# Performance work log

Measured on AMD Instinct MI355X. Metric: run time of the kernel, lower is better.

## Reference

```python
import jax, jax.numpy as jnp
import numpy as np

D = 2048        # dim
H = 16          # n_heads
FFN = 4 * D     # ffn hidden
K = 8192        # working-memory slots
HID = 32        # halt-gate hidden
EPS = 1e-5      # LayerNorm eps


def setup_inputs() -> dict:
    key = jax.random.key(0)
    ks = jax.random.split(key, 16)
    s = 0.02  # weight init scale for numerical sanity
    def rn(k, shape, scale=s):
        return jax.random.normal(k, shape, dtype=jnp.float32) * scale
    return {
        "workspace": jax.random.normal(ks[0], (D,), dtype=jnp.float32),
        "wm_context": jax.random.normal(ks[1], (K, D), dtype=jnp.float32),
        "self_in_w": rn(ks[2], (3 * D, D)), "self_in_b": jnp.zeros((3 * D,), jnp.float32),
        "self_out_w": rn(ks[3], (D, D)), "self_out_b": jnp.zeros((D,), jnp.float32),
        "cross_in_w": rn(ks[4], (3 * D, D)), "cross_in_b": jnp.zeros((3 * D,), jnp.float32),
        "cross_out_w": rn(ks[5], (D, D)), "cross_out_b": jnp.zeros((D,), jnp.float32),
        "ffn_w1": rn(ks[6], (FFN, D)), "ffn_b1": jnp.zeros((FFN,), jnp.float32),
        "ffn_w2": rn(ks[7], (D, FFN)), "ffn_b2": jnp.zeros((D,), jnp.float32),
        "ln1_g": jnp.ones((D,), jnp.float32), "ln1_b": jnp.zeros((D,), jnp.float32),
        "ln2_g": jnp.ones((D,), jnp.float32), "ln2_b": jnp.zeros((D,), jnp.float32),
        "ln3_g": jnp.ones((D,), jnp.float32), "ln3_b": jnp.zeros((D,), jnp.float32),
        "halt_w1": rn(ks[8], (HID, D)), "halt_b1": jnp.zeros((HID,), jnp.float32),
        "halt_w2": rn(ks[9], (1, HID)), "halt_b2": jnp.zeros((1,), jnp.float32),
        "max_steps": 5,
    }


def _ln(x, g, b):
    m = x.mean()
    v = jnp.mean((x - m) ** 2)
    return (x - m) / jnp.sqrt(v + EPS) * g + b


def _mha(xq, xkv, in_w, in_b, out_w, out_b):
    # xq: (D,) single query token; xkv: (L, D) keys/values. Eval mode (no dropout).
    d = xq.shape[-1]
    hd = d // H
    wq, wk, wv = in_w[:d], in_w[d:2 * d], in_w[2 * d:]
    bq, bk, bv = in_b[:d], in_b[d:2 * d], in_b[2 * d:]
    q = (xq @ wq.T + bq).reshape(H, hd)            # (H, hd)
    k = (xkv @ wk.T + bk).reshape(-1, H, hd)       # (L, H, hd)
    v = (xkv @ wv.T + bv).reshape(-1, H, hd)       # (L, H, hd)
    scores = jnp.einsum("hd,khd->hk", q, k) * (hd ** -0.5)  # (H, L)
    attn = jax.nn.softmax(scores, axis=-1)
    o = jnp.einsum("hk,khd->hd", attn, v).reshape(d)
    return o @ out_w.T + out_b


def reference(workspace, wm_context,
              self_in_w, self_in_b, self_out_w, self_out_b,
              cross_in_w, cross_in_b, cross_out_w, cross_out_b,
              ffn_w1, ffn_b1, ffn_w2, ffn_b2,
              ln1_g, ln1_b, ln2_g, ln2_b, ln3_g, ln3_b,
              halt_w1, halt_b1, halt_w2, halt_b2, max_steps):
    state = workspace
    cum = jnp.float32(0.0)
    acc = jnp.zeros_like(state)
    active = jnp.bool_(True)
    for _ in range(max_steps):  # fixed small loop over ACT steps
        cross = _mha(state, wm_context, cross_in_w, cross_in_b, cross_out_w, cross_out_b)
        s1 = _ln(state + cross, ln1_g, ln1_b)
        sa = _mha(s1, s1[None, :], self_in_w, self_in_b, self_out_w, self_out_b)
        s2 = _ln(s1 + sa, ln2_g, ln2_b)
        h = jax.nn.gelu(s2 @ ffn_w1.T + ffn_b1, approximate=False)
        new_state = _ln(s2 + (h @ ffn_w2.T + ffn_b2), ln3_g, ln3_b)
        hh = jax.nn.gelu(new_state @ halt_w1.T + halt_b1, approximate=False)
        halt = jax.nn.sigmoid(hh @ halt_w2.T + halt_b2)[0]
        new_cum = cum + halt
        halts = new_cum >= 1.0 - 1e-6
        # remainder = 1 - cum_before if halting, else halt_prob
        w = jnp.where(halts, 1.0 - cum, halt)
        acc = acc + jnp.where(active, w, 0.0) * new_state
        state = jnp.where(active, new_state, state)
        cum = jnp.where(active, new_cum, cum)
        active = jnp.logical_and(active, jnp.logical_not(halts))
    # if loop exhausted without halting, add leftover mass on last state
    acc = acc + jnp.where(cum < 1.0 - 1e-6, 1.0 - cum, 0.0) * state
    return acc
```

## Files before the change

kernel.cpp:

```cpp
#include <hip/hip_runtime.h>
#include <math.h>

#define DD 2048
#define NH 16
#define HDIM 128
#define NK 8192
#define NFFN 8192
#define NHID 32
#define EPSV 1e-5f

typedef __attribute__((ext_vector_type(8))) short bf16x8;
typedef __attribute__((ext_vector_type(4))) float f32x4;

static const size_t W_ST  = 0;
static const size_t W_AC  = 2048;
static const size_t W_SC  = 4096;
static const size_t W_Q   = 4160;
static const size_t W_T   = 6208;
static const size_t W_TB  = 38976;
static const size_t W_PS  = 55360;
static const size_t W_P   = 1103936;
static const size_t W_PB  = 1235008;
static const size_t W_U   = 1300544;
static const size_t W_O   = 1333312;
static const size_t W_CR  = 1335360;
static const size_t W_S1  = 1337408;
static const size_t W_V   = 1339456;
static const size_t W_SA  = 1341504;
static const size_t W_S2  = 1343552;
static const size_t W_H1  = 1345600;
static const size_t W_F2  = 1353792;
static const size_t W_NS  = 1355840;
static const size_t W_PUA = 1357888;
static const size_t W_PUB = 1882176;
static const size_t W_WMB = 1882176;
static const size_t W_WMT = 10270784;
static const size_t W_ENDA  = 18659392;
static const size_t W_ENDB  = 6076480;
static const size_t W_ENDB2 = 2930752;

__device__ __forceinline__ float gelu_exact(float x) {
  return 0.5f * x * (1.0f + erff(x * 0.70710678118654752f));
}
__device__ __forceinline__ unsigned short f2bf(float x) {
  unsigned u = __float_as_uint(x);
  u += 0x7FFFu + ((u >> 16) & 1u);
  return (unsigned short)(u >> 16);
}

__global__ void init_kernel(const float* __restrict__ w0, float* __restrict__ state,
                            float* __restrict__ acc, float* __restrict__ scal) {
  int i = blockIdx.x * 256 + threadIdx.x;
  if (i < DD) { state[i] = w0[i]; acc[i] = 0.f; }
  if (i == 0) { scal[0] = 0.f; scal[1] = 1.f; }
}

__global__ void prep_wm(const float* __restrict__ wm, unsigned short* __restrict__ wmb,
                        unsigned short* __restrict__ wmbT) {
  __shared__ unsigned short tile[64][72];
  int bk = blockIdx.x & 127, bc = blockIdx.x >> 7;
  int k0 = bk * 64, c0 = bc * 64;
  int tx = threadIdx.x & 15, ty = threadIdx.x >> 4;
#pragma unroll
  for (int rr = 0; rr < 4; ++rr) {
    int r = ty + rr * 16;
    float4 v = *reinterpret_cast<const float4*>(wm + (size_t)(k0 + r) * DD + c0 + tx * 4);
    ushort4 u4;
    u4.x = f2bf(v.x); u4.y = f2bf(v.y); u4.z = f2bf(v.z); u4.w = f2bf(v.w);
    *reinterpret_cast<ushort4*>(wmb + (size_t)(k0 + r) * DD + c0 + tx * 4) = u4;
    tile[tx * 4 + 0][r] = u4.x; tile[tx * 4 + 1][r] = u4.y;
    tile[tx * 4 + 2][r] = u4.z; tile[tx * 4 + 3][r] = u4.w;
  }
  __syncthreads();
#pragma unroll
  for (int rr = 0; rr < 4; ++rr) {
    int c = ty + rr * 16;
    ushort4 o;
    o.x = tile[c][tx * 4]; o.y = tile[c][tx * 4 + 1];
    o.z = tile[c][tx * 4 + 2]; o.w = tile[c][tx * 4 + 3];
    *reinterpret_cast<ushort4*>(wmbT + (size_t)(c0 + c) * NK + k0 + tx * 4) = o;
  }
}

__global__ void matvec_kernel(const float* __restrict__ W, const float* __restrict__ bias,
                              const float* __restrict__ x, float* __restrict__ y,
                              int R, int C, int act, int perhead,
                              const float* __restrict__ scal, int gated) {
  if (gated && scal[1] == 0.f) return;
  int wid = threadIdx.x >> 6, lane = threadIdx.x & 63;
  int row = blockIdx.x * 4 + wid;
  if (row >= R) return;
  const float* w = W + (size_t)row * C;
  const float* xv = perhead ? (x + (size_t)(row >> 7) * C) : x;
  float acc = 0.f;
  for (int c = lane * 4; c < C; c += 64 * 4) {
    float4 wv = *reinterpret_cast<const float4*>(w + c);
    float4 xx = *reinterpret_cast<const float4*>(xv + c);
    acc += wv.x * xx.x + wv.y * xx.y + wv.z * xx.z + wv.w * xx.w;
  }
  for (int off = 32; off > 0; off >>= 1) acc += __shfl_xor(acc, off, 64);
  if (lane == 0) {
    float r = acc + bias[row];
    if (act == 1) r = gelu_exact(r);
    y[row] = r;
  }
}

__global__ void tproj_kernel(const float* __restrict__ Wk, const float* __restrict__ q,
                             float* __restrict__ t, unsigned short* __restrict__ tb,
                             int obf, const float* __restrict__ scal) {
  if (scal[1] == 0.f) return;
  int h = blockIdx.x >> 4;
  int ct = blockIdx.x & 15;
  int c = ct * 128 + threadIdx.x;
  const float* wb = Wk + (size_t)(h * HDIM) * DD + c;
  const float* qh = q + h * HDIM;
  float acc = 0.f;
  for (int d = 0; d < HDIM; ++d) acc += qh[d] * wb[(size_t)d * DD];
  if (obf) tb[h * DD + c] = f2bf(acc);
  else     t[h * DD + c] = acc;
}

__global__ __launch_bounds__(256, 4) void scores_mfma(const unsigned short* __restrict__ wmb,
                                                      const unsigned short* __restrict__ tb,
                                                      float* __restrict__ part_s,
                                                      const float* __restrict__ scal) {
  if (scal[1] == 0.f) return;
  int w = threadIdx.x >> 6, lane = threadIdx.x & 63;
  int task = blockIdx.x * 4 + w;
  int cc = task & 7, rg = task >> 3;
  int r0 = rg * 16, c0 = cc * 256;
  int l15 = lane & 15, kg = lane >> 4;
  const unsigned short* ap = wmb + (size_t)(r0 + l15) * DD + c0 + kg * 8;
  const unsigned short* bp = tb + (size_t)l15 * DD + c0 + kg * 8;
  bf16x8 a[8], b[8];
#pragma unroll
  for (int i = 0; i < 8; ++i) {
    a[i] = *reinterpret_cast<const bf16x8*>(ap + i * 32);
    b[i] = *reinterpret_cast<const bf16x8*>(bp + i * 32);
  }
  f32x4 acc = {0.f, 0.f, 0.f, 0.f};
#pragma unroll
  for (int i = 0; i < 8; ++i)
    acc = __builtin_amdgcn_mfma_f32_16x16x32_bf16(a[i], b[i], acc, 0, 0, 0);
  float* op = part_s + ((size_t)cc * NH + l15) * NK + r0 + kg * 4;
#pragma unroll
  for (int r = 0; r < 4; ++r) op[r] = acc[r];
}

__global__ __launch_bounds__(256, 4) void u_mfma(const unsigned short* __restrict__ wmbT,
                                                 const unsigned short* __restrict__ pb,
                                                 float* __restrict__ part_u,
                                                 const float* __restrict__ scal) {
  if (scal[1] == 0.f) return;
  int w = threadIdx.x >> 6, lane = threadIdx.x & 63;
  int task = blockIdx.x * 4 + w;
  int ct = task & 127, kc = task >> 7;
  int c0 = ct * 16, k0 = kc * 512;
  int l15 = lane & 15, kg = lane >> 4;
  const unsigned short* ap = pb + (size_t)l15 * NK + k0 + kg * 8;
  const unsigned short* bp = wmbT + (size_t)(c0 + l15) * NK + k0 + kg * 8;
  f32x4 acc = {0.f, 0.f, 0.f, 0.f};
#pragma unroll
  for (int half = 0; half < 2; ++half) {
    bf16x8 a[8], b[8];
#pragma unroll
    for (int i = 0; i < 8; ++i) {
      a[i] = *reinterpret_cast<const bf16x8*>(ap + half * 256 + i * 32);
      b[i] = *reinterpret_cast<const bf16x8*>(bp + half * 256 + i * 32);
    }
#pragma unroll
    for (int i = 0; i < 8; ++i)
      acc = __builtin_amdgcn_mfma_f32_16x16x32_bf16(a[i], b[i], acc, 0, 0, 0);
  }
  float* op = part_u + ((size_t)kc * NH + kg * 4) * DD + c0 + l15;
#pragma unroll
  for (int r = 0; r < 4; ++r) op[(size_t)r * DD] = acc[r];
}

#define FMA16(wvv, tp)                                                       \
  {                                                                          \
    float4 t0 = tp[0], t1 = tp[1], t2 = tp[2], t3 = tp[3];                   \
    acc[0] += wvv * t0.x; acc[1] += wvv * t0.y;                              \
    acc[2] += wvv * t0.z; acc[3] += wvv * t0.w;                              \
    acc[4] += wvv * t1.x; acc[5] += wvv * t1.y;                              \
    acc[6] += wvv * t1.z; acc[7] += wvv * t1.w;                              \
    acc[8] += wvv * t2.x; acc[9] += wvv * t2.y;                              \
    acc[10] += wvv * t2.z; acc[11] += wvv * t2.w;                            \
    acc[12] += wvv * t3.x; acc[13] += wvv * t3.y;                            \
    acc[14] += wvv * t3.z; acc[15] += wvv * t3.w;                            \
  }

__global__ void scores_kernel(const float* __restrict__ wm, const float* __restrict__ t,
                              float* __restrict__ part_s, const float* __restrict__ scal) {
  if (scal[1] == 0.f) return;
  int kt = blockIdx.x >> 3;
  int cc = blockIdx.x & 7;
  int tid = threadIdx.x;
  int k0 = kt * 128, c0 = cc * 256;
  __shared__ float wlds[128 * 33];
  __shared__ float tlds[256 * 20];
  for (int j = 0; j < 32; ++j) {
    int idx = j * 128 + tid;
    int h = idx >> 8, c = idx & 255;
    tlds[c * 20 + h] = t[(size_t)h * DD + c0 + c];
  }
  float acc[NH];
#pragma unroll
  for (int h = 0; h < NH; ++h) acc[h] = 0.f;
  for (int s = 0; s < 8; ++s) {
    int cbase = c0 + s * 32;
    __syncthreads();
    for (int p = 0; p < 8; ++p) {
      int f = p * 128 + tid;
      int r = f >> 3, fc = f & 7;
      float4 v = *reinterpret_cast<const float4*>(wm + (size_t)(k0 + r) * DD + cbase + fc * 4);
      float* d = wlds + r * 33 + fc * 4;
      d[0] = v.x; d[1] = v.y; d[2] = v.z; d[3] = v.w;
    }
    __syncthreads();
    const float* myrow = wlds + tid * 33;
#pragma unroll 4
    for (int cb = 0; cb < 32; ++cb) {
      float wvv = myrow[cb];
      const float4* tp = reinterpret_cast<const float4*>(tlds + (size_t)(s * 32 + cb) * 20);
      FMA16(wvv, tp);
    }
  }
#pragma unroll
  for (int h = 0; h < NH; ++h)
    part_s[((size_t)cc * NH + h) * NK + k0 + tid] = acc[h];
}

__global__ void softmax_kernel(const float* __restrict__ part_s, float* __restrict__ p,
                               unsigned short* __restrict__ pb, int obf,
                               const float* __restrict__ scal) {
  if (scal[1] == 0.f) return;
  int h = blockIdx.x;
  int tid = threadIdx.x;
  __shared__ float red[256];
  float v[32];
  float mx = -1e30f;
  for (int j = 0; j < 32; ++j) {
    int k = tid + j * 256;
    float s = 0.f;
    for (int cc = 0; cc < 8; ++cc) s += part_s[((size_t)cc * NH + h) * NK + k];
    s *= 0.08838834764831845f;
    v[j] = s;
    mx = fmaxf(mx, s);
  }
  red[tid] = mx; __syncthreads();
  for (int off = 128; off > 0; off >>= 1) { if (tid < off) red[tid] = fmaxf(red[tid], red[tid + off]); __syncthreads(); }
  mx = red[0]; __syncthreads();
  float sum = 0.f;
  for (int j = 0; j < 32; ++j) { v[j] = expf(v[j] - mx); sum += v[j]; }
  red[tid] = sum; __syncthreads();
  for (int off = 128; off > 0; off >>= 1) { if (tid < off) red[tid] += red[tid + off]; __syncthreads(); }
  float inv = 1.f / red[0];
  for (int j = 0; j < 32; ++j) {
    float val = v[j] * inv;
    size_t idx = (size_t)h * NK + tid + j * 256;
    if (obf) pb[idx] = f2bf(val);
    else     p[idx] = val;
  }
}

#define U1FMA(i, ph) \
  acc[i].x += w4.x * (ph); acc[i].y += w4.y * (ph); \
  acc[i].z += w4.z * (ph); acc[i].w += w4.w * (ph);

template <int KCH>
__global__ void u1_kernel(const float* __restrict__ wm, const float* __restrict__ p,
                          float* __restrict__ part_u, const float* __restrict__ scal) {
  if (scal[1] == 0.f) return;
  int kc = blockIdx.x >> 2;
  int ct = blockIdx.x & 3;
  int tid = threadIdx.x;
  int k0 = kc * KCH;
  int c = ct * 512 + tid * 4;
  __shared__ float plds[KCH * 16];
  for (int j = 0; j < KCH * 16 / 128; ++j) {
    int idx = j * 128 + tid;
    int h = idx / KCH, k = idx % KCH;
    plds[k * 16 + h] = p[(size_t)h * NK + k0 + k];
  }
  __syncthreads();
  float4 acc[NH];
#pragma unroll
  for (int h = 0; h < NH; ++h) acc[h] = make_float4(0.f, 0.f, 0.f, 0.f);
#pragma unroll 2
  for (int k = 0; k < KCH; ++k) {
    float4 w4 = *reinterpret_cast<const float4*>(wm + (size_t)(k0 + k) * DD + c);
    const float4* pp = reinterpret_cast<const float4*>(plds + k * 16);
    float4 p0 = pp[0], p1 = pp[1], p2 = pp[2], p3 = pp[3];
    U1FMA(0, p0.x)  U1FMA(1, p0.y)  U1FMA(2, p0.z)  U1FMA(3, p0.w)
    U1FMA(4, p1.x)  U1FMA(5, p1.y)  U1FMA(6, p1.z)  U1FMA(7, p1.w)
    U1FMA(8, p2.x)  U1FMA(9, p2.y)  U1FMA(10, p2.z) U1FMA(11, p2.w)
    U1FMA(12, p3.x) U1FMA(13, p3.y) U1FMA(14, p3.z) U1FMA(15, p3.w)
  }
#pragma unroll
  for (int h = 0; h < NH; ++h)
    *reinterpret_cast<float4*>(part_u + ((size_t)kc * NH + h) * DD + c) = acc[h];
}

__global__ void u2_kernel(const float* __restrict__ part_u, float* __restrict__ u,
                          const float* __restrict__ scal, int nkc) {
  if (scal[1] == 0.f) return;
  int i = blockIdx.x * 256 + threadIdx.x;
  float s = 0.f;
  for (int kc = 0; kc < nkc; ++kc) s += part_u[(size_t)kc * NH * DD + i];
  u[i] = s;
}

__global__ void ln_kernel(const float* __restrict__ a, const float* __restrict__ r,
                          const float* __restrict__ g, const float* __restrict__ beta,
                          float* __restrict__ out, const float* __restrict__ scal) {
  if (scal[1] == 0.f) return;
  __shared__ float red[256];
  __shared__ float mv[2];
  int tid = threadIdx.x;
  float x[8];
  float s = 0.f;
  for (int j = 0; j < 8; ++j) { int i = tid * 8 + j; x[j] = a[i] + r[i]; s += x[j]; }
  red[tid] = s; __syncthreads();
  for (int off = 128; off > 0; off >>= 1) { if (tid < off) red[tid] += red[tid + off]; __syncthreads(); }
  if (tid == 0) mv[0] = red[0] * (1.f / DD);
  __syncthreads();
  float m = mv[0];
  s = 0.f;
  for (int j = 0; j < 8; ++j) { float d = x[j] - m; s += d * d; }
  red[tid] = s; __syncthreads();
  for (int off = 128; off > 0; off >>= 1) { if (tid < off) red[tid] += red[tid + off]; __syncthreads(); }
  if (tid == 0) mv[1] = 1.f / sqrtf(red[0] * (1.f / DD) + EPSV);
  __syncthreads();
  float inv = mv[1];
  for (int j = 0; j < 8; ++j) { int i = tid * 8 + j; out[i] = (x[j] - m) * inv * g[i] + beta[i]; }
}

__global__ void act_kernel(const float* __restrict__ hw1, const float* __restrict__ hb1,
                           const float* __restrict__ hw2, const float* __restrict__ hb2,
                           const float* __restrict__ ns, float* __restrict__ state,
                           float* __restrict__ acc, float* __restrict__ scal,
                           const int* __restrict__ max_steps, int step) {
  if (step >= max_steps[0]) return;
  if (scal[1] == 0.f) return;
  __shared__ float red[NHID][9];
  __shared__ float hh[NHID];
  __shared__ float wbc;
  int tid = threadIdx.x;
  int row = tid >> 3, seg = tid & 7;
  const float* wr = hw1 + (size_t)row * DD + seg * 256;
  const float* nsp = ns + seg * 256;
  float s = 0.f;
  for (int i = 0; i < 256; ++i) s += wr[i] * nsp[i];
  red[row][seg] = s; __syncthreads();
  if (tid < NHID) {
    float t = hb1[tid];
    for (int j = 0; j < 8; ++j) t += red[tid][j];
    hh[tid] = gelu_exact(t);
  }
  __syncthreads();
  if (tid == 0) {
    float hs = hb2[0];
    for (int j = 0; j < NHID; ++j) hs += hh[j] * hw2[j];
    float halt = 1.f / (1.f + expf(-hs));
    float cum = scal[0];
    float ncum = cum + halt;
    int halts = (ncum >= 1.f - 1e-6f);
    wbc = halts ? (1.f - cum) : halt;
    scal[0] = ncum;
    scal[1] = halts ? 0.f : 1.f;
  }
  __syncthreads();
  float w = wbc;
  for (int i = tid; i < DD; i += 256) {
    acc[i] += w * ns[i];
    state[i] = ns[i];
  }
}

__global__ void final_kernel(const float* __restrict__ state, const float* __restrict__ acc,
                             const float* __restrict__ scal, float* __restrict__ out) {
  float cum = scal[0];
  float w = (cum < 1.f - 1e-6f) ? (1.f - cum) : 0.f;
  int i = blockIdx.x * 256 + threadIdx.x;
  if (i < DD) out[i] = acc[i] + w * state[i];
}

extern "C" void kernel_launch(void* const* d_in, const int* in_sizes, int n_in,
                              void* d_out, int out_size, void* d_ws, size_t ws_size,
                              hipStream_t stream) {
  const float* workspace   = (const float*)d_in[0];
  const float* wm          = (const float*)d_in[1];
  const float* self_in_w   = (const float*)d_in[2];
  const float* self_in_b   = (const float*)d_in[3];
  const float* self_out_w  = (const float*)d_in[4];
  const float* self_out_b  = (const float*)d_in[5];
  const float* cross_in_w  = (const float*)d_in[6];
  const float* cross_in_b  = (const float*)d_in[7];
  const float* cross_out_w = (const float*)d_in[8];
  const float* cross_out_b = (const float*)d_in[9];
  const float* ffn_w1      = (const float*)d_in[10];
  const float* ffn_b1      = (const float*)d_in[11];
  const float* ffn_w2      = (const float*)d_in[12];
  const float* ffn_b2      = (const float*)d_in[13];
  const float* ln1_g = (const float*)d_in[14];
  const float* ln1_b = (const float*)d_in[15];
  const float* ln2_g = (const float*)d_in[16];
  const float* ln2_b = (const float*)d_in[17];
  const float* ln3_g = (const float*)d_in[18];
  const float* ln3_b = (const float*)d_in[19];
  const float* halt_w1 = (const float*)d_in[20];
  const float* halt_b1 = (const float*)d_in[21];
  const float* halt_w2 = (const float*)d_in[22];
  const float* halt_b2 = (const float*)d_in[23];
  const int*   max_steps = (const int*)d_in[24];

  float* ws = (float*)d_ws;
  float* out = (float*)d_out;

  float* ST = ws + W_ST;  float* AC = ws + W_AC;  float* SC = ws + W_SC;
  float* Q_ = ws + W_Q;   float* T_ = ws + W_T;   float* PS = ws + W_PS;
  float* P_ = ws + W_P;   float* U_ = ws + W_U;   float* O_ = ws + W_O;
  float* CR = ws + W_CR;  float* S1 = ws + W_S1;  float* V_ = ws + W_V;
  float* SA = ws + W_SA;  float* S2 = ws + W_S2;  float* H1 = ws + W_H1;
  float* F2 = ws + W_F2;  float* NS = ws + W_NS;
  float* PUA = ws + W_PUA;
  float* PUB = ws + W_PUB;
  unsigned short* TB  = (unsigned short*)(ws + W_TB);
  unsigned short* PB  = (unsigned short*)(ws + W_PB);
  unsigned short* WMB = (unsigned short*)(ws + W_WMB);
  unsigned short* WMT = (unsigned short*)(ws + W_WMT);

  const bool tierA = W_ENDA * sizeof(float) <= ws_size;
  const bool bigB  = W_ENDB * sizeof(float) <= ws_size;

  init_kernel<<<8, 256, 0, stream>>>(workspace, ST, AC, SC);
  if (tierA) prep_wm<<<4096, 256, 0, stream>>>(wm, WMB, WMT);

  for (int s = 0; s < 5; ++s) {
    matvec_kernel<<<512, 256, 0, stream>>>(cross_in_w, cross_in_b, ST, Q_, DD, DD, 0, 0, SC, 1);
    tproj_kernel<<<256, 128, 0, stream>>>(cross_in_w + (size_t)DD * DD, Q_, T_, TB,
                                          tierA ? 1 : 0, SC);
    if (tierA) {
      scores_mfma<<<1024, 256, 0, stream>>>(WMB, TB, PS, SC);
      softmax_kernel<<<16, 256, 0, stream>>>(PS, P_, PB, 1, SC);
      u_mfma<<<512, 256, 0, stream>>>(WMT, PB, PUA, SC);
      u2_kernel<<<128, 256, 0, stream>>>(PUA, U_, SC, 16);
    } else {
      scores_kernel<<<512, 128, 0, stream>>>(wm, T_, PS, SC);
      softmax_kernel<<<16, 256, 0, stream>>>(PS, P_, PB, 0, SC);
      if (bigB) u1_kernel<64><<<512, 128, 0, stream>>>(wm, P_, PUB, SC);
      else      u1_kernel<256><<<128, 128, 0, stream>>>(wm, P_, PUB, SC);
      u2_kernel<<<128, 256, 0, stream>>>(PUB, U_, SC, bigB ? 128 : 32);
    }
    matvec_kernel<<<512, 256, 0, stream>>>(cross_in_w + (size_t)2 * DD * DD, cross_in_b + 2 * DD,
                                           U_, O_, DD, DD, 0, 1, SC, 1);
    matvec_kernel<<<512, 256, 0, stream>>>(cross_out_w, cross_out_b, O_, CR, DD, DD, 0, 0, SC, 1);
    ln_kernel<<<1, 256, 0, stream>>>(ST, CR, ln1_g, ln1_b, S1, SC);
    matvec_kernel<<<512, 256, 0, stream>>>(self_in_w + (size_t)2 * DD * DD, self_in_b + 2 * DD,
                                           S1, V_, DD, DD, 0, 0, SC, 1);
    matvec_kernel<<<512, 256, 0, stream>>>(self_out_w, self_out_b, V_, SA, DD, DD, 0, 0, SC, 1);
    ln_kernel<<<1, 256, 0, stream>>>(S1, SA, ln2_g, ln2_b, S2, SC);
    matvec_kernel<<<2048, 256, 0, stream>>>(ffn_w1, ffn_b1, S2, H1, NFFN, DD, 1, 0, SC, 1);
    matvec_kernel<<<512, 256, 0, stream>>>(ffn_w2, ffn_b2, H1, F2, DD, NFFN, 0, 0, SC, 1);
    ln_kernel<<<1, 256, 0, stream>>>(S2, F2, ln3_g, ln3_b, NS, SC);
    act_kernel<<<1, 256, 0, stream>>>(halt_w1, halt_b1, halt_w2, halt_b2, NS, ST, AC, SC,
                                      max_steps, s);
  }
  final_kernel<<<8, 256, 0, stream>>>(ST, AC, SC, out);
}
```

Baseline: 413.7 us.

## Fuse LayerNorms and partial-sum reductions into neighbouring matvec kernels

```diff
diff --git a/kernel.cpp b/kernel.cpp
--- a/kernel.cpp
+++ b/kernel.cpp
@@ -37,7 +37,6 @@
 static const size_t W_WMT = 10270784;
 static const size_t W_ENDA  = 18659392;
 static const size_t W_ENDB  = 6076480;
-static const size_t W_ENDB2 = 2930752;
 
 __device__ __forceinline__ float gelu_exact(float x) {
   return 0.5f * x * (1.0f + erff(x * 0.70710678118654752f));
@@ -46,6 +45,46 @@
   unsigned u = __float_as_uint(x);
   u += 0x7FFFu + ((u >> 16) & 1u);
   return (unsigned short)(u >> 16);
+}
+
+__device__ __forceinline__ float wave_dot(const float* __restrict__ w, const float* x, int C) {
+  int lane = threadIdx.x & 63;
+  float acc = 0.f;
+  for (int c = lane * 4; c < C; c += 256) {
+    float4 wv = *reinterpret_cast<const float4*>(w + c);
+    float4 xx = *reinterpret_cast<const float4*>(x + c);
+    acc += wv.x * xx.x + wv.y * xx.y + wv.z * xx.z + wv.w * xx.w;
+  }
+#pragma unroll
+  for (int off = 32; off; off >>= 1) acc += __shfl_xor(acc, off, 64);
+  return acc;
+}
+
+__device__ void block_ln(const float* x1, const float* x2,
+                         const float* __restrict__ g, const float* __restrict__ be,
+                         float* o, float* red) {
+  int tid = threadIdx.x;
+  float loc[8]; float s = 0.f;
+#pragma unroll
+  for (int j = 0; j < 8; ++j) { int i = tid * 8 + j; float v = x1[i] + x2[i]; loc[j] = v; s += v; }
+#pragma unroll
+  for (int off = 32; off; off >>= 1) s += __shfl_xor(s, off, 64);
+  __syncthreads();
+  if ((tid & 63) == 0) red[tid >> 6] = s;
+  __syncthreads();
+  float m = (red[0] + red[1] + red[2] + red[3]) * (1.f / 2048.f);
+  s = 0.f;
+#pragma unroll
+  for (int j = 0; j < 8; ++j) { float d = loc[j] - m; s += d * d; }
+#pragma unroll
+  for (int off = 32; off; off >>= 1) s += __shfl_xor(s, off, 64);
+  __syncthreads();
+  if ((tid & 63) == 0) red[tid >> 6] = s;
+  __syncthreads();
+  float inv = 1.f / sqrtf((red[0] + red[1] + red[2] + red[3]) * (1.f / 2048.f) + EPSV);
+#pragma unroll
+  for (int j = 0; j < 8; ++j) { int i = tid * 8 + j; o[i] = (loc[j] - m) * inv * g[i] + be[i]; }
+  __syncthreads();
 }
 
 __global__ void init_kernel(const float* __restrict__ w0, float* __restrict__ state,
@@ -93,7 +132,7 @@
   const float* w = W + (size_t)row * C;
   const float* xv = perhead ? (x + (size_t)(row >> 7) * C) : x;
   float acc = 0.f;
-  for (int c = lane * 4; c < C; c += 64 * 4) {
+  for (int c = lane * 4; c < C; c += 256) {
     float4 wv = *reinterpret_cast<const float4*>(w + c);
     float4 xx = *reinterpret_cast<const float4*>(xv + c);
     acc += wv.x * xx.x + wv.y * xx.y + wv.z * xx.z + wv.w * xx.w;
@@ -110,8 +149,7 @@
                              float* __restrict__ t, unsigned short* __restrict__ tb,
                              int obf, const float* __restrict__ scal) {
   if (scal[1] == 0.f) return;
-  int h = blockIdx.x >> 4;
-  int ct = blockIdx.x & 15;
+  int h = blockIdx.x >> 4, ct = blockIdx.x & 15;
   int c = ct * 128 + threadIdx.x;
   const float* wb = Wk + (size_t)(h * HDIM) * DD + c;
   const float* qh = q + h * HDIM;
@@ -177,6 +215,161 @@
 #pragma unroll
   for (int r = 0; r < 4; ++r) op[(size_t)r * DD] = acc[r];
 }
+
+__global__ void softmax_kernel(const float* __restrict__ part_s, float* __restrict__ p,
+                               unsigned short* __restrict__ pb, int obf,
+                               const float* __restrict__ scal) {
+  if (scal[1] == 0.f) return;
+  int h = blockIdx.x, tid = threadIdx.x;
+  __shared__ float red[256];
+  float v[32]; float mx = -1e30f;
+  for (int j = 0; j < 32; ++j) {
+    int k = tid + j * 256; float s = 0.f;
+    for (int cc = 0; cc < 8; ++cc) s += part_s[((size_t)cc * NH + h) * NK + k];
+    s *= 0.08838834764831845f;
+    v[j] = s; mx = fmaxf(mx, s);
+  }
+  red[tid] = mx; __syncthreads();
+  for (int off = 128; off > 0; off >>= 1) { if (tid < off) red[tid] = fmaxf(red[tid], red[tid + off]); __syncthreads(); }
+  mx = red[0]; __syncthreads();
+  float sum = 0.f;
+  for (int j = 0; j < 32; ++j) { v[j] = expf(v[j] - mx); sum += v[j]; }
+  red[tid] = sum; __syncthreads();
+  for (int off = 128; off > 0; off >>= 1) { if (tid < off) red[tid] += red[tid + off]; __syncthreads(); }
+  float inv = 1.f / red[0];
+  for (int j = 0; j < 32; ++j) {
+    float val = v[j] * inv;
+    size_t idx = (size_t)h * NK + tid + j * 256;
+    if (obf) pb[idx] = f2bf(val);
+    else     p[idx] = val;
+  }
+}
+
+__global__ __launch_bounds__(256) void o_fused_kernel(const float* __restrict__ part_u,
+                                                      const float* __restrict__ Wv,
+                                                      const float* __restrict__ bv,
+                                                      float* __restrict__ O,
+                                                      const float* __restrict__ scal) {
+  if (scal[1] == 0.f) return;
+  __shared__ float uh[2048];
+  int tid = threadIdx.x, wid = tid >> 6, lane = tid & 63;
+  int h = blockIdx.x >> 5;
+#pragma unroll
+  for (int j = 0; j < 8; ++j) {
+    int c = tid + j * 256;
+    float ss = 0.f;
+#pragma unroll
+    for (int kc = 0; kc < 16; ++kc) ss += part_u[((size_t)kc * NH + h) * DD + c];
+    uh[c] = ss;
+  }
+  __syncthreads();
+  int row = h * HDIM + (blockIdx.x & 31) * 4 + wid;
+  float a = wave_dot(Wv + (size_t)row * DD, uh, DD);
+  if (lane == 0) O[row] = a + bv[row];
+}
+
+__global__ __launch_bounds__(256) void v_ln1_kernel(const float* __restrict__ ST,
+                                                    const float* __restrict__ CR,
+                                                    const float* __restrict__ g1,
+                                                    const float* __restrict__ b1,
+                                                    const float* __restrict__ W,
+                                                    const float* __restrict__ bias,
+                                                    float* __restrict__ V,
+                                                    const float* __restrict__ scal) {
+  if (scal[1] == 0.f) return;
+  __shared__ float s1[2048];
+  __shared__ float red[8];
+  block_ln(ST, CR, g1, b1, s1, red);
+  int wid = threadIdx.x >> 6, lane = threadIdx.x & 63;
+  int row = blockIdx.x * 4 + wid;
+  float a = wave_dot(W + (size_t)row * DD, s1, DD);
+  if (lane == 0) V[row] = a + bias[row];
+}
+
+__global__ __launch_bounds__(256) void ffn1_kernel(const float* __restrict__ ST,
+                                                   const float* __restrict__ CR,
+                                                   const float* __restrict__ SA,
+                                                   const float* __restrict__ g1,
+                                                   const float* __restrict__ b1,
+                                                   const float* __restrict__ g2,
+                                                   const float* __restrict__ b2,
+                                                   const float* __restrict__ W,
+                                                   const float* __restrict__ bias,
+                                                   float* __restrict__ H1,
+                                                   const float* __restrict__ scal) {
+  if (scal[1] == 0.f) return;
+  __shared__ float s1[2048];
+  __shared__ float s2[2048];
+  __shared__ float red[8];
+  block_ln(ST, CR, g1, b1, s1, red);
+  block_ln(s1, SA, g2, b2, s2, red);
+  int wid = threadIdx.x >> 6, lane = threadIdx.x & 63;
+  int gw = blockIdx.x * 4 + wid;
+  for (int r = gw; r < NFFN; r += 2048) {
+    float a = wave_dot(W + (size_t)r * DD, s2, DD);
+    if (lane == 0) H1[r] = gelu_exact(a + bias[r]);
+  }
+}
+
+__global__ void act_ln3_kernel(const float* __restrict__ ST, const float* __restrict__ CR,
+                               const float* __restrict__ SA, const float* __restrict__ F2,
+                               const float* __restrict__ g1, const float* __restrict__ b1,
+                               const float* __restrict__ g2, const float* __restrict__ b2,
+                               const float* __restrict__ g3, const float* __restrict__ b3,
+                               const float* __restrict__ hw1, const float* __restrict__ hb1,
+                               const float* __restrict__ hw2, const float* __restrict__ hb2,
+                               float* __restrict__ state, float* __restrict__ acc,
+                               float* __restrict__ scal, const int* __restrict__ max_steps,
+                               int step) {
+  if (step >= max_steps[0]) return;
+  if (scal[1] == 0.f) return;
+  __shared__ float sA[2048];
+  __shared__ float sB[2048];
+  __shared__ float red[8];
+  __shared__ float hh[NHID];
+  __shared__ float wbc;
+  int tid = threadIdx.x;
+  block_ln(ST, CR, g1, b1, sA, red);
+  block_ln(sA, SA, g2, b2, sB, red);
+  block_ln(sB, F2, g3, b3, sA, red);
+  int row = tid >> 3, seg = tid & 7;
+  const float* wr = hw1 + (size_t)row * DD + seg * 256;
+  const float* np = sA + seg * 256;
+  float s = 0.f;
+  for (int i = 0; i < 256; ++i) s += wr[i] * np[i];
+  sB[row * 8 + seg] = s;
+  __syncthreads();
+  if (tid < NHID) {
+    float t2 = hb1[tid];
+#pragma unroll
+    for (int j = 0; j < 8; ++j) t2 += sB[tid * 8 + j];
+    hh[tid] = gelu_exact(t2);
+  }
+  __syncthreads();
+  if (tid == 0) {
+    float hs = hb2[0];
+    for (int j = 0; j < NHID; ++j) hs += hh[j] * hw2[j];
+    float halt = 1.f / (1.f + expf(-hs));
+    float cum = scal[0];
+    float ncum = cum + halt;
+    int halts = (ncum >= 1.f - 1e-6f);
+    wbc = halts ? (1.f - cum) : halt;
+    scal[0] = ncum;
+    scal[1] = halts ? 0.f : 1.f;
+  }
+  __syncthreads();
+  float w = wbc;
+  for (int i = tid; i < DD; i += 256) { acc[i] += w * sA[i]; state[i] = sA[i]; }
+}
+
+__global__ void final_kernel(const float* __restrict__ state, const float* __restrict__ acc,
+                             const float* __restrict__ scal, float* __restrict__ out) {
+  float cum = scal[0];
+  float w = (cum < 1.f - 1e-6f) ? (1.f - cum) : 0.f;
+  int i = blockIdx.x * 256 + threadIdx.x;
+  if (i < DD) out[i] = acc[i] + w * state[i];
+}
+
 
 #define FMA16(wvv, tp)                                                       \
   {                                                                          \
@@ -194,8 +387,7 @@
 __global__ void scores_kernel(const float* __restrict__ wm, const float* __restrict__ t,
                               float* __restrict__ part_s, const float* __restrict__ scal) {
   if (scal[1] == 0.f) return;
-  int kt = blockIdx.x >> 3;
-  int cc = blockIdx.x & 7;
+  int kt = blockIdx.x >> 3, cc = blockIdx.x & 7;
   int tid = threadIdx.x;
   int k0 = kt * 128, c0 = cc * 256;
   __shared__ float wlds[128 * 33];
@@ -208,8 +400,8 @@
   float acc[NH];
 #pragma unroll
   for (int h = 0; h < NH; ++h) acc[h] = 0.f;
-  for (int s = 0; s < 8; ++s) {
-    int cbase = c0 + s * 32;
+  for (int sl = 0; sl < 8; ++sl) {
+    int cbase = c0 + sl * 32;
     __syncthreads();
     for (int p = 0; p < 8; ++p) {
       int f = p * 128 + tid;
@@ -223,46 +415,13 @@
 #pragma unroll 4
     for (int cb = 0; cb < 32; ++cb) {
       float wvv = myrow[cb];
-      const float4* tp = reinterpret_cast<const float4*>(tlds + (size_t)(s * 32 + cb) * 20);
+      const float4* tp = reinterpret_cast<const float4*>(tlds + (size_t)(sl * 32 + cb) * 20);
       FMA16(wvv, tp);
     }
   }
 #pragma unroll
   for (int h = 0; h < NH; ++h)
     part_s[((size_t)cc * NH + h) * NK + k0 + tid] = acc[h];
-}
-
-__global__ void softmax_kernel(const float* __restrict__ part_s, float* __restrict__ p,
-                               unsigned short* __restrict__ pb, int obf,
-                               const float* __restrict__ scal) {
-  if (scal[1] == 0.f) return;
-  int h = blockIdx.x;
-  int tid = threadIdx.x;
-  __shared__ float red[256];
-  float v[32];
-  float mx = -1e30f;
-  for (int j = 0; j < 32; ++j) {
-    int k = tid + j * 256;
-    float s = 0.f;
-    for (int cc = 0; cc < 8; ++cc) s += part_s[((size_t)cc * NH + h) * NK + k];
-    s *= 0.08838834764831845f;
-    v[j] = s;
-    mx = fmaxf(mx, s);
-  }
-  red[tid] = mx; __syncthreads();
-  for (int off = 128; off > 0; off >>= 1) { if (tid < off) red[tid] = fmaxf(red[tid], red[tid + off]); __syncthreads(); }
-  mx = red[0]; __syncthreads();
-  float sum = 0.f;
-  for (int j = 0; j < 32; ++j) { v[j] = expf(v[j] - mx); sum += v[j]; }
-  red[tid] = sum; __syncthreads();
-  for (int off = 128; off > 0; off >>= 1) { if (tid < off) red[tid] += red[tid + off]; __syncthreads(); }
-  float inv = 1.f / red[0];
-  for (int j = 0; j < 32; ++j) {
-    float val = v[j] * inv;
-    size_t idx = (size_t)h * NK + tid + j * 256;
-    if (obf) pb[idx] = f2bf(val);
-    else     p[idx] = val;
-  }
 }
 
 #define U1FMA(i, ph) \
@@ -273,8 +432,7 @@
 __global__ void u1_kernel(const float* __restrict__ wm, const float* __restrict__ p,
                           float* __restrict__ part_u, const float* __restrict__ scal) {
   if (scal[1] == 0.f) return;
-  int kc = blockIdx.x >> 2;
-  int ct = blockIdx.x & 3;
+  int kc = blockIdx.x >> 2, ct = blockIdx.x & 3;
   int tid = threadIdx.x;
   int k0 = kc * KCH;
   int c = ct * 512 + tid * 4;
@@ -319,15 +477,13 @@
   __shared__ float red[256];
   __shared__ float mv[2];
   int tid = threadIdx.x;
-  float x[8];
-  float s = 0.f;
+  float x[8]; float s = 0.f;
   for (int j = 0; j < 8; ++j) { int i = tid * 8 + j; x[j] = a[i] + r[i]; s += x[j]; }
   red[tid] = s; __syncthreads();
   for (int off = 128; off > 0; off >>= 1) { if (tid < off) red[tid] += red[tid + off]; __syncthreads(); }
   if (tid == 0) mv[0] = red[0] * (1.f / DD);
   __syncthreads();
-  float m = mv[0];
-  s = 0.f;
+  float m = mv[0]; s = 0.f;
   for (int j = 0; j < 8; ++j) { float d = x[j] - m; s += d * d; }
   red[tid] = s; __syncthreads();
   for (int off = 128; off > 0; off >>= 1) { if (tid < off) red[tid] += red[tid + off]; __syncthreads(); }
@@ -373,18 +529,7 @@
   }
   __syncthreads();
   float w = wbc;
-  for (int i = tid; i < DD; i += 256) {
-    acc[i] += w * ns[i];
-    state[i] = ns[i];
-  }
-}
-
-__global__ void final_kernel(const float* __restrict__ state, const float* __restrict__ acc,
-                             const float* __restrict__ scal, float* __restrict__ out) {
-  float cum = scal[0];
-  float w = (cum < 1.f - 1e-6f) ? (1.f - cum) : 0.f;
-  int i = blockIdx.x * 256 + threadIdx.x;
-  if (i < DD) out[i] = acc[i] + w * state[i];
+  for (int i = tid; i < DD; i += 256) { acc[i] += w * ns[i]; state[i] = ns[i]; }
 }
 
 extern "C" void kernel_launch(void* const* d_in, const int* in_sizes, int n_in,
@@ -420,53 +565,67 @@
   float* out = (float*)d_out;
 
   float* ST = ws + W_ST;  float* AC = ws + W_AC;  float* SC = ws + W_SC;
-  float* Q_ = ws + W_Q;   float* T_ = ws + W_T;   float* PS = ws + W_PS;
-  float* P_ = ws + W_P;   float* U_ = ws + W_U;   float* O_ = ws + W_O;
-  float* CR = ws + W_CR;  float* S1 = ws + W_S1;  float* V_ = ws + W_V;
-  float* SA = ws + W_SA;  float* S2 = ws + W_S2;  float* H1 = ws + W_H1;
-  float* F2 = ws + W_F2;  float* NS = ws + W_NS;
-  float* PUA = ws + W_PUA;
-  float* PUB = ws + W_PUB;
+  float* Q_ = ws + W_Q;   float* PS = ws + W_PS;  float* O_ = ws + W_O;
+  float* CR = ws + W_CR;  float* V_ = ws + W_V;   float* SA = ws + W_SA;
+  float* H1 = ws + W_H1;  float* F2 = ws + W_F2;  float* PU = ws + W_PUA;
   unsigned short* TB  = (unsigned short*)(ws + W_TB);
   unsigned short* PB  = (unsigned short*)(ws + W_PB);
   unsigned short* WMB = (unsigned short*)(ws + W_WMB);
   unsigned short* WMT = (unsigned short*)(ws + W_WMT);
 
   const bool tierA = W_ENDA * sizeof(float) <= ws_size;
-  const bool bigB  = W_ENDB * sizeof(float) <= ws_size;
 
   init_kernel<<<8, 256, 0, stream>>>(workspace, ST, AC, SC);
-  if (tierA) prep_wm<<<4096, 256, 0, stream>>>(wm, WMB, WMT);
-
-  for (int s = 0; s < 5; ++s) {
-    matvec_kernel<<<512, 256, 0, stream>>>(cross_in_w, cross_in_b, ST, Q_, DD, DD, 0, 0, SC, 1);
-    tproj_kernel<<<256, 128, 0, stream>>>(cross_in_w + (size_t)DD * DD, Q_, T_, TB,
-                                          tierA ? 1 : 0, SC);
-    if (tierA) {
+
+  if (tierA) {
+    prep_wm<<<4096, 256, 0, stream>>>(wm, WMB, WMT);
+    for (int s = 0; s < 5; ++s) {
+      matvec_kernel<<<512, 256, 0, stream>>>(cross_in_w, cross_in_b, ST, Q_, DD, DD, 0, 0, SC, 1);
+      tproj_kernel<<<256, 128, 0, stream>>>(cross_in_w + (size_t)DD * DD, Q_, nullptr, TB, 1, SC);
       scores_mfma<<<1024, 256, 0, stream>>>(WMB, TB, PS, SC);
-      softmax_kernel<<<16, 256, 0, stream>>>(PS, P_, PB, 1, SC);
-      u_mfma<<<512, 256, 0, stream>>>(WMT, PB, PUA, SC);
-      u2_kernel<<<128, 256, 0, stream>>>(PUA, U_, SC, 16);
-    } else {
+      softmax_kernel<<<16, 256, 0, stream>>>(PS, nullptr, PB, 1, SC);
+      u_mfma<<<512, 256, 0, stream>>>(WMT, PB, PU, SC);
+      o_fused_kernel<<<512, 256, 0, stream>>>(PU, cross_in_w + (size_t)2 * DD * DD,
+                                              cross_in_b + 2 * DD, O_, SC);
+      matvec_kernel<<<512, 256, 0, stream>>>(cross_out_w, cross_out_b, O_, CR, DD, DD, 0, 0, SC, 1);
+      v_ln1_kernel<<<512, 256, 0, stream>>>(ST, CR, ln1_g, ln1_b,
+                                            self_in_w + (size_t)2 * DD * DD,
+                                            self_in_b + 2 * DD, V_, SC);
+      matvec_kernel<<<512, 256, 0, stream>>>(self_out_w, self_out_b, V_, SA, DD, DD, 0, 0, SC, 1);
+      ffn1_kernel<<<512, 256, 0, stream>>>(ST, CR, SA, ln1_g, ln1_b, ln2_g, ln2_b,
+                                           ffn_w1, ffn_b1, H1, SC);
+      matvec_kernel<<<512, 256, 0, stream>>>(ffn_w2, ffn_b2, H1, F2, DD, NFFN, 0, 0, SC, 1);
+      act_ln3_kernel<<<1, 256, 0, stream>>>(ST, CR, SA, F2, ln1_g, ln1_b, ln2_g, ln2_b,
+                                            ln3_g, ln3_b, halt_w1, halt_b1, halt_w2, halt_b2,
+                                            ST, AC, SC, max_steps, s);
+    }
+  } else {
+    float* T_ = ws + W_T;   float* P_ = ws + W_P;   float* U_ = ws + W_U;
+    float* S1 = ws + W_S1;  float* S2 = ws + W_S2;  float* NS = ws + W_NS;
+    float* PUB = ws + W_PUB;
+    const bool bigB = W_ENDB * sizeof(float) <= ws_size;
+    for (int s = 0; s < 5; ++s) {
+      matvec_kernel<<<512, 256, 0, stream>>>(cross_in_w, cross_in_b, ST, Q_, DD, DD, 0, 0, SC, 1);
+      tproj_kernel<<<256, 128, 0, stream>>>(cross_in_w + (size_t)DD * DD, Q_, T_, nullptr, 0, SC);
       scores_kernel<<<512, 128, 0, stream>>>(wm, T_, PS, SC);
-      softmax_kernel<<<16, 256, 0, stream>>>(PS, P_, PB, 0, SC);
+      softmax_kernel<<<16, 256, 0, stream>>>(PS, P_, nullptr, 0, SC);
       if (bigB) u1_kernel<64><<<512, 128, 0, stream>>>(wm, P_, PUB, SC);
       else      u1_kernel<256><<<128, 128, 0, stream>>>(wm, P_, PUB, SC);
       u2_kernel<<<128, 256, 0, stream>>>(PUB, U_, SC, bigB ? 128 : 32);
+      matvec_kernel<<<512, 256, 0, stream>>>(cross_in_w + (size_t)2 * DD * DD, cross_in_b + 2 * DD,
+                                             U_, O_, DD, DD, 0, 1, SC, 1);
+      matvec_kernel<<<512, 256, 0, stream>>>(cross_out_w, cross_out_b, O_, CR, DD, DD, 0, 0, SC, 1);
+      ln_kernel<<<1, 256, 0, stream>>>(ST, CR, ln1_g, ln1_b, S1, SC);
+      matvec_kernel<<<512, 256, 0, stream>>>(self_in_w + (size_t)2 * DD * DD, self_in_b + 2 * DD,
+                                             S1, V_, DD, DD, 0, 0, SC, 1);
+      matvec_kernel<<<512, 256, 0, stream>>>(self_out_w, self_out_b, V_, SA, DD, DD, 0, 0, SC, 1);
+      ln_kernel<<<1, 256, 0, stream>>>(S1, SA, ln2_g, ln2_b, S2, SC);
+      matvec_kernel<<<2048, 256, 0, stream>>>(ffn_w1, ffn_b1, S2, H1, NFFN, DD, 1, 0, SC, 1);
+      matvec_kernel<<<512, 256, 0, stream>>>(ffn_w2, ffn_b2, H1, F2, DD, NFFN, 0, 0, SC, 1);
+      ln_kernel<<<1, 256, 0, stream>>>(S2, F2, ln3_g, ln3_b, NS, SC);
+      act_kernel<<<1, 256, 0, stream>>>(halt_w1, halt_b1, halt_w2, halt_b2, NS, ST, AC, SC,
+                                        max_steps, s);
     }
-    matvec_kernel<<<512, 256, 0, stream>>>(cross_in_w + (size_t)2 * DD * DD, cross_in_b + 2 * DD,
-                                           U_, O_, DD, DD, 0, 1, SC, 1);
-    matvec_kernel<<<512, 256, 0, stream>>>(cross_out_w, cross_out_b, O_, CR, DD, DD, 0, 0, SC, 1);
-    ln_kernel<<<1, 256, 0, stream>>>(ST, CR, ln1_g, ln1_b, S1, SC);
-    matvec_kernel<<<512, 256, 0, stream>>>(self_in_w + (size_t)2 * DD * DD, self_in_b + 2 * DD,
-                                           S1, V_, DD, DD, 0, 0, SC, 1);
-    matvec_kernel<<<512, 256, 0, stream>>>(self_out_w, self_out_b, V_, SA, DD, DD, 0, 0, SC, 1);
-    ln_kernel<<<1, 256, 0, stream>>>(S1, SA, ln2_g, ln2_b, S2, SC);
-    matvec_kernel<<<2048, 256, 0, stream>>>(ffn_w1, ffn_b1, S2, H1, NFFN, DD, 1, 0, SC, 1);
-    matvec_kernel<<<512, 256, 0, stream>>>(ffn_w2, ffn_b2, H1, F2, DD, NFFN, 0, 0, SC, 1);
-    ln_kernel<<<1, 256, 0, stream>>>(S2, F2, ln3_g, ln3_b, NS, SC);
-    act_kernel<<<1, 256, 0, stream>>>(halt_w1, halt_b1, halt_w2, halt_b2, NS, ST, AC, SC,
-                                      max_steps, s);
   }
   final_kernel<<<8, 256, 0, stream>>>(ST, AC, SC, out);
 }
```

After: 368.1 us. -11.0%, faster.
